# Performance work log

Hardware: AMD Instinct MI355X
Metric: run time of the kernel (lower is better)

## Reference

```python
import jax, jax.numpy as jnp
import numpy as np

M = 500000  # inner reduction dim per group; 4 groups x 21 outputs = 84 rows of tmp


def setup_inputs() -> dict:
    key = jax.random.key(0)
    ks = jax.random.split(key, 5)
    probs_params = jnp.array([
        [1.8134, 1.6573, -0.2452, 1.8745],
        [2.6430, 1.5442, -0.0449, 1.5576],
        [2.8379, 1.4989, 0.0158, 1.4974],
        [2.9666, 1.4671, 0.0577, 1.4586],
        [3.0934, 1.4350, 0.1002, 1.4213],
    ], dtype=jnp.float32)
    return {
        "BEV": jax.random.normal(ks[0], (1,), jnp.float32),
        "ST0": jax.random.normal(ks[1], (4, M), jnp.float32),
        "Weight0": jax.random.normal(ks[2], (4, M, 21), jnp.float32),
        "ST1": jax.random.normal(ks[3], (4, M), jnp.float32),
        "Weight1": jax.random.normal(ks[4], (4, M, 21), jnp.float32),
        "probs_params": probs_params,          # the 5 probsK nn.Parameters stacked
        "BEV_p": jnp.float32(0.2058),           # self.BEV parameter
        "B": jnp.float32(0.3089),               # self.B parameter
    }


def calc_probs(p):
    # p: softmaxed 4-vector. Reproduces the nested-loop ordering:
    # for i: [p_i, for j: [p_i*p_j, for k: p_i*p_j*p_k]] -> 84 entries.
    o2 = p[:, None] * p[None, :]                  # (4,4)   p_i*p_j
    o3 = o2[:, :, None] * p[None, None, :]        # (4,4,4) p_i*p_j*p_k
    block = jnp.concatenate([o2[:, :, None], o3], axis=2)       # (4,4,5)
    per_i = jnp.concatenate([p[:, None], block.reshape(4, 20)], axis=1)  # (4,21)
    return per_i.reshape(-1)                      # (84,)


def reference(BEV, ST0, Weight0, ST1, Weight1, probs_params, BEV_p, B):
    # (5,84) -- calc_probs of softmax of each of the 5 parameter vectors
    P = jax.vmap(calc_probs)(jax.nn.softmax(probs_params, axis=-1))
    base = jax.nn.relu(BEV_p) * BEV[0]            # scalar, broadcast over ST
    sig0 = jax.nn.sigmoid(B * (base + ST0))       # (4, M)
    sig1 = jax.nn.sigmoid(B * (base + ST1))       # (4, M)
    # per-group matvec sigmoid(.) @ Weight[i], concatenated -> (84,)
    tmp0 = jnp.einsum('im,imp->ip', sig0, Weight0).reshape(-1)
    tmp1 = jnp.einsum('im,imp->ip', sig1, Weight1).reshape(-1)
    outs = jnp.concatenate([(P[0] @ tmp0)[None], P[1:] @ tmp1])  # (5,)
    return jnp.mean(outs)
```

## Files before the change

### kernel.cpp

```cpp
#include <hip/hip_runtime.h>
#include <hip/hip_bf16.h>

typedef float f32x4 __attribute__((ext_vector_type(4)));

#define M_DIM   500000
#define NPER    21
#define NELEM   (M_DIM * NPER)
#define NF4     (NELEM / 4)
#define NBLK    256
#define TPB     252
#define CH      2
#define STR_F4  (NBLK * TPB * CH)
#define DM      ((STR_F4 * 4) / 21)
#define P_PIN   12
#define P_FULL  20

__device__ __forceinline__ float sig_fast(float st, float k1, float k0) {
    return __builtin_amdgcn_rcpf(1.0f + __builtin_amdgcn_exp2f(fmaf(st, k1, k0)));
}

__global__ __launch_bounds__(TPB) void probs_reduce_kernel(
    const float* __restrict__ ST0, const float* __restrict__ W0,
    const float* __restrict__ ST1, const float* __restrict__ W1,
    const float* __restrict__ BEV, const float* __restrict__ BEVp,
    const float* __restrict__ Bp, float* __restrict__ tmp)
{
    const int t   = threadIdx.x;
    const int tau = blockIdx.y >> 2;
    const int grp = blockIdx.y & 3;

    const float* __restrict__ ST = (tau == 0 ? ST0 : ST1) + grp * M_DIM;
    const float* __restrict__ Wg = (tau == 0 ? W0 : W1) + (size_t)grp * NELEM;

    const float B    = Bp[0];
    const float base = fmaxf(BEVp[0], 0.0f) * BEV[0];
    const float k1   = -B * 1.44269504f;
    const float k0   = k1 * base;

    int c0 = (blockIdx.x * TPB + t) * CH;
    const int e0 = c0 * 4;
    int m = (int)((unsigned)e0 / 21u);
    const int cthr = 21 - (e0 - m * 21);

    float a0=0.f,a1=0.f,a2=0.f,a3=0.f,a4=0.f,a5=0.f,a6=0.f,a7=0.f;

#define BODY(LOADA, LOADB)                                              \
    {                                                                   \
        const f32x4 wA = LOADA;                                         \
        const f32x4 wB = LOADB;                                         \
        const int   mp = (m + 1 < M_DIM) ? m + 1 : M_DIM - 1;           \
        const float g0 = sig_fast(ST[m],  k1, k0);                      \
        const float g1 = sig_fast(ST[mp], k1, k0);                      \
        a0 = fmaf(wA[0], g0, a0);                                       \
        a1 = fmaf(wA[1], (1 < cthr) ? g0 : g1, a1);                     \
        a2 = fmaf(wA[2], (2 < cthr) ? g0 : g1, a2);                     \
        a3 = fmaf(wA[3], (3 < cthr) ? g0 : g1, a3);                     \
        a4 = fmaf(wB[0], (4 < cthr) ? g0 : g1, a4);                     \
        a5 = fmaf(wB[1], (5 < cthr) ? g0 : g1, a5);                     \
        a6 = fmaf(wB[2], (6 < cthr) ? g0 : g1, a6);                     \
        a7 = fmaf(wB[3], (7 < cthr) ? g0 : g1, a7);                     \
    }

    #pragma unroll 1
    for (int p = 0; p < P_PIN; ++p) {
        const f32x4* wp = (const f32x4*)(Wg + (size_t)c0 * 4);
        BODY(wp[0], wp[1]);
        c0 += STR_F4; m += DM;
    }
    #pragma unroll 1
    for (int p = P_PIN; p < P_FULL; ++p) {
        const f32x4* wp = (const f32x4*)(Wg + (size_t)c0 * 4);
        BODY(__builtin_nontemporal_load(wp), __builtin_nontemporal_load(wp + 1));
        c0 += STR_F4; m += DM;
    }
    if (c0 < NF4) {
        const f32x4* wp = (const f32x4*)(Wg + (size_t)c0 * 4);
        BODY(__builtin_nontemporal_load(wp), __builtin_nontemporal_load(wp + 1));
    }
#undef BODY

    __shared__ float sm[TPB * 8];
    sm[t*8+0]=a0; sm[t*8+1]=a1; sm[t*8+2]=a2; sm[t*8+3]=a3;
    sm[t*8+4]=a4; sm[t*8+5]=a5; sm[t*8+6]=a6; sm[t*8+7]=a7;
    __syncthreads();

    if (t < NPER) {
        float s = 0.f;
        #pragma unroll
        for (int q = 0; q < (TPB * 8) / NPER; ++q)
            s += sm[t + NPER * q];
        atomicAdd(&tmp[blockIdx.y * NPER + t], s);
    }
}

__global__ void probs_final_kernel(const float* __restrict__ tmp,
                                   const float* __restrict__ pp,
                                   float* __restrict__ out)
{
    __shared__ float red[128];
    const int t = threadIdx.x;
    float val = 0.f;
    if (t < 84) {
        const int i = t / 21, inner = t % 21;
        float Pk[5];
        #pragma unroll
        for (int k = 0; k < 5; ++k) {
            float a0 = pp[k*4+0], a1 = pp[k*4+1], a2 = pp[k*4+2], a3 = pp[k*4+3];
            float mx = fmaxf(fmaxf(a0, a1), fmaxf(a2, a3));
            float e0 = __expf(a0-mx), e1 = __expf(a1-mx), e2 = __expf(a2-mx), e3 = __expf(a3-mx);
            float inv = 1.0f / (e0 + e1 + e2 + e3);
            float q[4] = {e0*inv, e1*inv, e2*inv, e3*inv};
            float v = q[i];
            if (inner > 0) {
                int jj = (inner - 1) / 5, kk = (inner - 1) % 5;
                v *= q[jj];
                if (kk > 0) v *= q[kk - 1];
            }
            Pk[k] = v;
        }
        float t0 = tmp[t], t1 = tmp[84 + t];
        val = Pk[0] * t0 + (Pk[1] + Pk[2] + Pk[3] + Pk[4]) * t1;
    }
    red[t] = val;
    __syncthreads();
    #pragma unroll
    for (int s = 64; s > 0; s >>= 1) {
        if (t < s) red[t] += red[t + s];
        __syncthreads();
    }
    if (t == 0) out[0] = red[0] * 0.2f;
}

extern "C" void kernel_launch(void* const* d_in, const int* in_sizes, int n_in,
                              void* d_out, int out_size, void* d_ws, size_t ws_size,
                              hipStream_t stream) {
    const float* BEV  = (const float*)d_in[0];
    const float* ST0  = (const float*)d_in[1];
    const float* W0   = (const float*)d_in[2];
    const float* ST1  = (const float*)d_in[3];
    const float* W1   = (const float*)d_in[4];
    const float* pp   = (const float*)d_in[5];
    const float* BEVp = (const float*)d_in[6];
    const float* B    = (const float*)d_in[7];
    float* out = (float*)d_out;
    float* tmp = (float*)d_ws;

    hipMemsetAsync(tmp, 0, 168 * sizeof(float), stream);
    probs_reduce_kernel<<<dim3(NBLK, 8), TPB, 0, stream>>>(ST0, W0, ST1, W1,
                                                           BEV, BEVp, B, tmp);
    probs_final_kernel<<<1, 128, 0, stream>>>(tmp, pp, out);
}
```

Before: 70.65 us.

## Replace atomics and memset with per-block partials reduced in final kernel

Each reduce block now writes its 21 partial sums to a distinct workspace slot instead of issuing atomicAdd into a shared 168-entry buffer. This removes the hipMemsetAsync launch and the atomic contention. The final kernel now sums the 256 partials per row itself before the probability-weighted reduction. The change also drops the split between cached and nontemporal weight loads, so all weight loads use plain loads. The cost is a serial 256-element loop per thread in the single-block final kernel.

```diff
diff --git a/kernel.cpp b/kernel.cpp
--- a/kernel.cpp
+++ b/kernel.cpp
@@ -7,12 +7,11 @@
 #define NPER    21
 #define NELEM   (M_DIM * NPER)
 #define NF4     (NELEM / 4)
-#define NBLK    256
+#define NBX     256
 #define TPB     252
 #define CH      2
-#define STR_F4  (NBLK * TPB * CH)
+#define STR_F4  (NBX * TPB * CH)
 #define DM      ((STR_F4 * 4) / 21)
-#define P_PIN   12
 #define P_FULL  20
 
 __device__ __forceinline__ float sig_fast(float st, float k1, float k0) {
@@ -23,7 +22,7 @@
     const float* __restrict__ ST0, const float* __restrict__ W0,
     const float* __restrict__ ST1, const float* __restrict__ W1,
     const float* __restrict__ BEV, const float* __restrict__ BEVp,
-    const float* __restrict__ Bp, float* __restrict__ tmp)
+    const float* __restrict__ Bp, float* __restrict__ partial)
 {
     const int t   = threadIdx.x;
     const int tau = blockIdx.y >> 2;
@@ -44,10 +43,11 @@
 
     float a0=0.f,a1=0.f,a2=0.f,a3=0.f,a4=0.f,a5=0.f,a6=0.f,a7=0.f;
 
-#define BODY(LOADA, LOADB)                                              \
+#define BODY()                                                          \
     {                                                                   \
-        const f32x4 wA = LOADA;                                         \
-        const f32x4 wB = LOADB;                                         \
+        const f32x4* wp = (const f32x4*)(Wg + (size_t)c0 * 4);          \
+        const f32x4 wA = wp[0];                                         \
+        const f32x4 wB = wp[1];                                         \
         const int   mp = (m + 1 < M_DIM) ? m + 1 : M_DIM - 1;           \
         const float g0 = sig_fast(ST[m],  k1, k0);                      \
         const float g1 = sig_fast(ST[mp], k1, k0);                      \
@@ -62,20 +62,12 @@
     }
 
     #pragma unroll 1
-    for (int p = 0; p < P_PIN; ++p) {
-        const f32x4* wp = (const f32x4*)(Wg + (size_t)c0 * 4);
-        BODY(wp[0], wp[1]);
-        c0 += STR_F4; m += DM;
-    }
-    #pragma unroll 1
-    for (int p = P_PIN; p < P_FULL; ++p) {
-        const f32x4* wp = (const f32x4*)(Wg + (size_t)c0 * 4);
-        BODY(__builtin_nontemporal_load(wp), __builtin_nontemporal_load(wp + 1));
+    for (int p = 0; p < P_FULL; ++p) {
+        BODY();
         c0 += STR_F4; m += DM;
     }
     if (c0 < NF4) {
-        const f32x4* wp = (const f32x4*)(Wg + (size_t)c0 * 4);
-        BODY(__builtin_nontemporal_load(wp), __builtin_nontemporal_load(wp + 1));
+        BODY();
     }
 #undef BODY
 
@@ -89,16 +81,29 @@
         #pragma unroll
         for (int q = 0; q < (TPB * 8) / NPER; ++q)
             s += sm[t + NPER * q];
-        atomicAdd(&tmp[blockIdx.y * NPER + t], s);
+        partial[(blockIdx.y * NBX + blockIdx.x) * NPER + t] = s;
     }
 }
 
-__global__ void probs_final_kernel(const float* __restrict__ tmp,
-                                   const float* __restrict__ pp,
-                                   float* __restrict__ out)
+__global__ __launch_bounds__(256) void probs_final_kernel(
+    const float* __restrict__ partial,
+    const float* __restrict__ pp,
+    float* __restrict__ out)
 {
-    __shared__ float red[128];
+    __shared__ float tmpL[168];
+    __shared__ float red[256];
     const int t = threadIdx.x;
+
+    if (t < 168) {
+        const int y = t / NPER, p = t % NPER;
+        float s = 0.f;
+        #pragma unroll 4
+        for (int bx = 0; bx < NBX; ++bx)
+            s += partial[(y * NBX + bx) * NPER + p];
+        tmpL[y * NPER + p] = s;
+    }
+    __syncthreads();
+
     float val = 0.f;
     if (t < 84) {
         const int i = t / 21, inner = t % 21;
@@ -118,13 +123,13 @@
             }
             Pk[k] = v;
         }
-        float t0 = tmp[t], t1 = tmp[84 + t];
+        float t0 = tmpL[t], t1 = tmpL[84 + t];
         val = Pk[0] * t0 + (Pk[1] + Pk[2] + Pk[3] + Pk[4]) * t1;
     }
     red[t] = val;
     __syncthreads();
     #pragma unroll
-    for (int s = 64; s > 0; s >>= 1) {
+    for (int s = 128; s > 0; s >>= 1) {
         if (t < s) red[t] += red[t + s];
         __syncthreads();
     }
@@ -143,10 +148,9 @@
     const float* BEVp = (const float*)d_in[6];
     const float* B    = (const float*)d_in[7];
     float* out = (float*)d_out;
-    float* tmp = (float*)d_ws;
+    float* partial = (float*)d_ws;
 
-    hipMemsetAsync(tmp, 0, 168 * sizeof(float), stream);
-    probs_reduce_kernel<<<dim3(NBLK, 8), TPB, 0, stream>>>(ST0, W0, ST1, W1,
-                                                           BEV, BEVp, B, tmp);
-    probs_final_kernel<<<1, 128, 0, stream>>>(tmp, pp, out);
+    probs_reduce_kernel<<<dim3(NBX, 8), TPB, 0, stream>>>(ST0, W0, ST1, W1,
+                                                          BEV, BEVp, B, partial);
+    probs_final_kernel<<<1, 256, 0, stream>>>(partial, pp, out);
 }
```

Measured after the change: 87.51 us. 1.24x slower.
